# Kernel optimization log

Measured on AMD Instinct MI355X. Metric: run time of the kernel, lower is better.

## Reference

```python
import jax, jax.numpy as jnp
import numpy as np

N_NODES = 50000
N_REL = 3
N_EDGES = 800000
D_FEAT = 128
D_HID = 128  # == dim_embs so residual + concat dims line up
D_QUERY = 64


def setup_inputs() -> dict:
    key = jax.random.key(0)
    ks = jax.random.split(key, 8)
    s = 1.0 / np.sqrt(D_HID)
    return {
        "x": jax.random.normal(ks[0], (N_NODES, D_FEAT), dtype=jnp.float32),
        "edges": jax.random.randint(ks[1], (N_REL, 2, N_EDGES), 0, N_NODES, dtype=jnp.int64),
        "feat_w": jax.random.normal(ks[2], (D_FEAT, D_HID), dtype=jnp.float32) * s,
        "conv_w": jax.random.normal(ks[3], (2, N_REL, D_HID, D_HID), dtype=jnp.float32) * s,
        "conv_b": jax.random.normal(ks[4], (2, N_REL, D_HID), dtype=jnp.float32) * 0.01,
        "attn_w": jax.random.normal(ks[5], (2, D_HID, D_QUERY), dtype=jnp.float32) * s,
        "attn_q": jax.random.normal(ks[6], (2, D_QUERY), dtype=jnp.float32) * s,
        "concat_w": jax.random.normal(ks[7], (D_HID, 3 * D_HID), dtype=jnp.float32) * s,
    }


def reference(x, edges, feat_w, conv_w, conv_b, attn_w, attn_q, concat_w):
    N = x.shape[0]
    R = edges.shape[0]
    ones_e = jnp.ones((edges.shape[2],), dtype=x.dtype)

    def gconv(h, src, dst, W, b):
        # GraphConv with symmetric ('both') normalization + residual
        deg_out = jnp.clip(jax.ops.segment_sum(ones_e, src, num_segments=N), 1.0)
        deg_in = jnp.clip(jax.ops.segment_sum(ones_e, dst, num_segments=N), 1.0)
        m = (h * jax.lax.rsqrt(deg_out)[:, None]) @ W          # [N, D]
        agg = jax.ops.segment_sum(m[src], dst, num_segments=N)  # gather-scatter [E, D] -> [N, D]
        return agg * jax.lax.rsqrt(deg_in)[:, None] + b + h

    def het_layer(h, l):
        # per-relation conv, then attention-weighted aggregation across relations
        vals = jnp.stack([gconv(h, edges[r, 0], edges[r, 1], conv_w[l, r], conv_b[l, r])
                          for r in range(R)])                   # [R, N, D]
        keys = jnp.tanh(jnp.einsum('rnd,dq->rnq', vals, attn_w[l]))
        scores = jnp.einsum('rnq,q->rn', keys, attn_q[l])       # [R, N]
        attn = jax.nn.softmax(scores, axis=0)                   # softmax over relations
        return jnp.einsum('rn,rnd->nd', attn, vals), attn

    h0 = jnp.tanh(x @ feat_w)            # feature_trans + tanh
    h1, _ = het_layer(h0, 1)             # 1-hop path (convs[1] only)
    t, _ = het_layer(h0, 0)              # 2-hop path: convs[0]
    h2, attn = het_layer(t, 1)           # then convs[1]
    y = jnp.concatenate([h0, h1, h2], axis=-1) @ concat_w.T  # concat_weight (no bias)
    return y, attn.T                      # attn_res: [N, R]
```

## Files before the change

kernel.cpp:

```cpp
#include <hip/hip_runtime.h>

#define NN 50000
#define NE 800000
#define DD 128
#define DQ 64
#define NB 42
#define SL 19048
#define NW 25000

typedef __attribute__((ext_vector_type(8))) short short8_t;
typedef __attribute__((ext_vector_type(4))) float f32x4;

__device__ __forceinline__ int clampi(int v, int lo, int hi) {
  return v < lo ? lo : (v > hi ? hi : v);
}
__device__ __forceinline__ unsigned short f2bf(float f) {
  unsigned int u = __float_as_uint(f);
  return (unsigned short)((u + 0x7FFFu + ((u >> 16) & 1u)) >> 16);
}
__device__ __forceinline__ float bfl(unsigned int u) { return __uint_as_float(u << 16); }
__device__ __forceinline__ float bfh(unsigned int u) { return __uint_as_float(u & 0xFFFF0000u); }
__device__ __forceinline__ float b2f(short s) {
  return __uint_as_float(((unsigned int)(unsigned short)s) << 16);
}

__global__ void detect_kernel(const int* __restrict__ e, int* __restrict__ flag) {
  if (threadIdx.x == 0 && blockIdx.x == 0) {
    int f = 1;
    for (int j = 0; j < 32; ++j)
      if (e[2 * j + 1] != 0) f = 0;
    *flag = f;
  }
}

__global__ __launch_bounds__(512) void hist6_kernel(
    const int* __restrict__ e, const int* __restrict__ flag,
    unsigned int* __restrict__ hist) {
  __shared__ unsigned int lds[NW];
  const int b = blockIdx.x;
  const int c = blockIdx.y;
  const int r = c >> 1;
  const int a = c & 1;
  const int tid = threadIdx.x;
  const int f = *flag;
  for (int i = tid; i < NW; i += 512) lds[i] = 0u;
  __syncthreads();
  const long long abase = (long long)r * 2 * NE + (a ? 0 : NE);
  const int beg = b * SL, end = min(beg + SL, NE);
  for (int i = beg + tid; i < end; i += 512) {
    int v = clampi(e[(abase + i) << f], 0, NN - 1);
    atomicAdd(&lds[v >> 1], 1u << ((v & 1) * 16));
  }
  __syncthreads();
  unsigned int* outp = hist + ((size_t)c * NB + b) * NW;
  for (int i = tid; i < NW; i += 512) outp[i] = lds[i];
}

__global__ __launch_bounds__(256) void sumhist_kernel(
    const unsigned int* __restrict__ hist, int* __restrict__ cnt,
    float* __restrict__ rsqi, float* __restrict__ rsqo) {
  const int c = blockIdx.y;
  const int r = c >> 1;
  const int a = c & 1;
  for (int wl = threadIdx.x; wl < 1000; wl += 256) {
    int w = blockIdx.x * 1000 + wl;
    unsigned int lo = 0, hi = 0;
    const unsigned int* hp = hist + (size_t)c * NB * NW + w;
#pragma unroll 7
    for (int b = 0; b < NB; ++b) {
      unsigned int v = hp[(size_t)b * NW];
      lo += v & 0xFFFFu;
      hi += v >> 16;
    }
    int n0 = 2 * w, n1 = 2 * w + 1;
    if (a == 0) {
      cnt[r * NN + n0] = (int)lo;
      cnt[r * NN + n1] = (int)hi;
      rsqi[r * NN + n0] = rsqrtf(fmaxf((float)lo, 1.0f));
      rsqi[r * NN + n1] = rsqrtf(fmaxf((float)hi, 1.0f));
    } else {
      rsqo[r * NN + n0] = rsqrtf(fmaxf((float)lo, 1.0f));
      rsqo[r * NN + n1] = rsqrtf(fmaxf((float)hi, 1.0f));
    }
  }
}

__global__ __launch_bounds__(256) void scanp1_kernel(
    const int* __restrict__ cnt, int* __restrict__ rowptr, int* __restrict__ btot) {
  __shared__ int part[256];
  const int r = blockIdx.y;
  const int b = blockIdx.x;
  const int t = threadIdx.x;
  const int base = b * 2000;
  const int beg = t * 8;
  int v[8];
  int s = 0;
  if (beg < 2000) {
#pragma unroll
    for (int j = 0; j < 8; ++j) {
      v[j] = cnt[r * NN + base + beg + j];
      s += v[j];
    }
  }
  part[t] = s;
  __syncthreads();
  for (int off = 1; off < 256; off <<= 1) {
    int x = (t >= off) ? part[t - off] : 0;
    __syncthreads();
    part[t] += x;
    __syncthreads();
  }
  if (beg < 2000) {
    int excl = part[t] - s;
#pragma unroll
    for (int j = 0; j < 8; ++j) {
      rowptr[r * (NN + 1) + base + beg + j] = excl;
      excl += v[j];
    }
  }
  if (t == 255) btot[r * 25 + b] = part[255];
}

__global__ __launch_bounds__(64) void scanp2_kernel(
    const int* __restrict__ btot, int* __restrict__ boff, int* __restrict__ rowptr) {
  if (threadIdx.x == 0) {
    for (int r = 0; r < 3; ++r) {
      int run = 0;
      for (int b = 0; b < 25; ++b) {
        boff[r * 25 + b] = run;
        run += btot[r * 25 + b];
      }
      rowptr[r * (NN + 1) + NN] = run;
    }
  }
}

__global__ __launch_bounds__(256) void scanp3_kernel(
    const int* __restrict__ boff, int* __restrict__ rowptr) {
  const int r = blockIdx.y, b = blockIdx.x, t = threadIdx.x;
  const int off = boff[r * 25 + b];
  const int beg = t * 8;
  if (beg < 2000) {
    int* rp = rowptr + r * (NN + 1) + b * 2000 + beg;
#pragma unroll
    for (int j = 0; j < 8; ++j) rp[j] += off;
  }
}

__global__ __launch_bounds__(256) void bases_kernel(
    const unsigned int* __restrict__ hist, const int* __restrict__ rowptr,
    int* __restrict__ bases) {
  const int r = blockIdx.y;
  for (int wl = threadIdx.x; wl < 1000; wl += 256) {
    int w = blockIdx.x * 1000 + wl;
    int n0 = 2 * w, n1 = 2 * w + 1;
    int run0 = rowptr[r * (NN + 1) + n0];
    int run1 = rowptr[r * (NN + 1) + n1];
    const unsigned int* hp = hist + (size_t)(r * 2) * NB * NW + w;
    int* bp = bases + (size_t)r * NB * NN;
#pragma unroll 7
    for (int b = 0; b < NB; ++b) {
      unsigned int v = hp[(size_t)b * NW];
      bp[(size_t)b * NN + n0] = run0;
      bp[(size_t)b * NN + n1] = run1;
      run0 += (int)(v & 0xFFFFu);
      run1 += (int)(v >> 16);
    }
  }
}

__global__ __launch_bounds__(512) void fill2_kernel(
    const int* __restrict__ e, const int* __restrict__ flag,
    const int* __restrict__ bases, int* __restrict__ col) {
  __shared__ unsigned int cur[NW];
  const int b = blockIdx.x;
  const int r = blockIdx.y;
  const int tid = threadIdx.x;
  const int f = *flag;
  for (int i = tid; i < NW; i += 512) cur[i] = 0u;
  __syncthreads();
  const long long sbase = (long long)r * 2 * NE;
  const int beg = b * SL, end = min(beg + SL, NE);
  const int* bp = bases + ((size_t)r * NB + b) * NN;
  for (int i = beg + tid; i < end; i += 512) {
    int s = clampi(e[(sbase + i) << f], 0, NN - 1);
    int d = clampi(e[(sbase + NE + i) << f], 0, NN - 1);
    unsigned int packed = atomicAdd(&cur[d >> 1], 1u << ((d & 1) * 16));
    int local = (int)((packed >> ((d & 1) * 16)) & 0xFFFFu);
    int pos = clampi(bp[d] + local, 0, NE - 1);
    col[(size_t)r * NE + pos] = s;
  }
}

__global__ __launch_bounds__(256) void prepw_kernel(
    const float* __restrict__ conv_w, const float* __restrict__ feat_w,
    const float* __restrict__ concat_w, const float* __restrict__ attn_w,
    unsigned short* __restrict__ fw) {
  const int i = blockIdx.x;
  if (i < 10) {
    unsigned short* dst = fw + (size_t)i * 16384;
    for (int e = threadIdx.x; e < 2048; e += 256) {
      int nt = e >> 8, ks = (e >> 6) & 3, lane = e & 63;
      int n = (lane & 15) + nt * 16;
      int kb = (lane >> 4) * 8 + ks * 32;
      unsigned int w[4];
#pragma unroll
      for (int jj = 0; jj < 4; ++jj) {
        int k0 = kb + 2 * jj, k1 = k0 + 1;
        float f0, f1;
        if (i < 6) {
          f0 = conv_w[(size_t)i * 16384 + (size_t)k0 * DD + n];
          f1 = conv_w[(size_t)i * 16384 + (size_t)k1 * DD + n];
        } else if (i == 6) {
          f0 = feat_w[(size_t)k0 * DD + n];
          f1 = feat_w[(size_t)k1 * DD + n];
        } else {
          int p = i - 7;
          f0 = concat_w[(size_t)n * 384 + p * DD + k0];
          f1 = concat_w[(size_t)n * 384 + p * DD + k1];
        }
        w[jj] = (unsigned int)f2bf(f0) | ((unsigned int)f2bf(f1) << 16);
      }
      ((uint4*)dst)[e] = make_uint4(w[0], w[1], w[2], w[3]);
    }
  } else {
    const int l = i - 10;
    unsigned short* dst = fw + (size_t)10 * 16384 + (size_t)l * 8192;
    for (int e = threadIdx.x; e < 1024; e += 256) {
      int nt = e >> 8, ks = (e >> 6) & 3, lane = e & 63;
      int n = (lane & 15) + nt * 16;
      int kb = (lane >> 4) * 8 + ks * 32;
      unsigned int w[4];
#pragma unroll
      for (int jj = 0; jj < 4; ++jj) {
        int k0 = kb + 2 * jj, k1 = k0 + 1;
        float f0 = attn_w[((size_t)l * DD + k0) * DQ + n];
        float f1 = attn_w[((size_t)l * DD + k1) * DQ + n];
        w[jj] = (unsigned int)f2bf(f0) | ((unsigned int)f2bf(f1) << 16);
      }
      ((uint4*)dst)[e] = make_uint4(w[0], w[1], w[2], w[3]);
    }
  }
}

template <int AFP32, int TANH, int EPI, int SIX>
__global__ __launch_bounds__(256) void mgemm_kernel(
    const void* __restrict__ Ap, const unsigned short* __restrict__ fw,
    const float* __restrict__ rsqi, const float* __restrict__ bias,
    const unsigned short* __restrict__ residb, unsigned short* __restrict__ Cb) {
  const size_t ND = (size_t)NN * DD;
  const int rel = blockIdx.y;
  const int wsel = SIX ? (rel + 3) % 6 : rel;
  const int arel = SIX ? rel % 3 : rel;
  const unsigned short* fwp = fw + (size_t)wsel * 16384;
  const float* rsqip = EPI ? rsqi + (size_t)arel * NN : nullptr;
  const float* biasp = EPI ? bias + (size_t)wsel * DD : nullptr;
  unsigned short* Cbp = Cb + (size_t)rel * ND;
  __shared__ unsigned short sF[16384];
  const int tid = threadIdx.x;
  {
    const float4* s = (const float4*)fwp;
    float4* d = (float4*)sF;
#pragma unroll
    for (int i = 0; i < 8; ++i) d[tid + i * 256] = s[tid + i * 256];
  }
  __syncthreads();
  const int w = tid >> 6, l = tid & 63, la = l & 15, gr = l >> 4;
  const int row0 = blockIdx.x * 128 + w * 32;
  if (row0 >= NN) return;
  const bool m1ok = (row0 + 32) <= NN;
  short8_t a[2][4];
#pragma unroll
  for (int m = 0; m < 2; ++m) {
    const int r = row0 + m * 16 + la;
    const bool ok = (m == 0) || m1ok;
    if (AFP32) {
      const float* ap = (const float*)Ap + (size_t)r * DD + gr * 8;
#pragma unroll
      for (int ks = 0; ks < 4; ++ks) {
        short8_t v = (short8_t)0;
        if (ok) {
          float4 x0 = *(const float4*)(ap + ks * 32);
          float4 x1 = *(const float4*)(ap + ks * 32 + 4);
          v[0] = (short)f2bf(x0.x); v[1] = (short)f2bf(x0.y);
          v[2] = (short)f2bf(x0.z); v[3] = (short)f2bf(x0.w);
          v[4] = (short)f2bf(x1.x); v[5] = (short)f2bf(x1.y);
          v[6] = (short)f2bf(x1.z); v[7] = (short)f2bf(x1.w);
        }
        a[m][ks] = v;
      }
    } else {
      const unsigned short* ap =
          (const unsigned short*)Ap + (size_t)arel * ND + (size_t)r * DD + gr * 8;
#pragma unroll
      for (int ks = 0; ks < 4; ++ks)
        a[m][ks] = ok ? *(const short8_t*)(ap + ks * 32) : (short8_t)0;
    }
  }
  f32x4 zero = {0.f, 0.f, 0.f, 0.f};
  f32x4 acc[2][8];
#pragma unroll
  for (int m = 0; m < 2; ++m)
#pragma unroll
    for (int nt = 0; nt < 8; ++nt) acc[m][nt] = zero;
#pragma unroll
  for (int nt = 0; nt < 8; ++nt) {
#pragma unroll
    for (int ks = 0; ks < 4; ++ks) {
      short8_t b = *(const short8_t*)(sF + ((nt * 4 + ks) * 64 + l) * 8);
      acc[0][nt] = __builtin_amdgcn_mfma_f32_16x16x32_bf16(a[0][ks], b, acc[0][nt], 0, 0, 0);
      acc[1][nt] = __builtin_amdgcn_mfma_f32_16x16x32_bf16(a[1][ks], b, acc[1][nt], 0, 0, 0);
    }
  }
#pragma unroll
  for (int m = 0; m < 2; ++m) {
    if (m == 1 && !m1ok) break;
#pragma unroll
    for (int rr = 0; rr < 4; ++rr) {
      const int row = row0 + m * 16 + gr * 4 + rr;
      const float sc = EPI ? rsqip[row] : 0.0f;
#pragma unroll
      for (int nt = 0; nt < 8; ++nt) {
        const int c0 = nt * 16 + la;
        float v = acc[m][nt][rr];
        if (TANH) v = tanhf(v);
        if (EPI) {
          float rv = __uint_as_float((unsigned int)residb[(size_t)row * DD + c0] << 16);
          v = fmaf(v, sc, biasp[c0] + rv);
        }
        Cbp[(size_t)row * DD + c0] = f2bf(v);
      }
    }
  }
}

__global__ __launch_bounds__(512) void mconcat_kernel(
    const unsigned short* __restrict__ h0b, const unsigned short* __restrict__ h1b,
    const unsigned short* __restrict__ h2b, const unsigned short* __restrict__ fwc,
    float* __restrict__ Y) {
  __shared__ unsigned short sF[3 * 16384];
  const int tid = threadIdx.x;
  {
    const float4* s = (const float4*)fwc;
    float4* d = (float4*)sF;
#pragma unroll
    for (int i = 0; i < 12; ++i) d[tid + i * 512] = s[tid + i * 512];
  }
  __syncthreads();
  const int w = tid >> 6, l = tid & 63, la = l & 15, gr = l >> 4;
  const int row0 = blockIdx.x * 256 + w * 32;
  if (row0 >= NN) return;
  const bool m1ok = (row0 + 32) <= NN;
  const unsigned short* hb[3] = {h0b, h1b, h2b};
  f32x4 zero = {0.f, 0.f, 0.f, 0.f};
  f32x4 acc[2][8];
#pragma unroll
  for (int m = 0; m < 2; ++m)
#pragma unroll
    for (int nt = 0; nt < 8; ++nt) acc[m][nt] = zero;
#pragma unroll
  for (int p = 0; p < 3; ++p) {
    short8_t a[2][4];
#pragma unroll
    for (int m = 0; m < 2; ++m) {
      const int r = row0 + m * 16 + la;
      const bool ok = (m == 0) || m1ok;
      const unsigned short* ap = hb[p] + (size_t)r * DD + gr * 8;
#pragma unroll
      for (int ks = 0; ks < 4; ++ks)
        a[m][ks] = ok ? *(const short8_t*)(ap + ks * 32) : (short8_t)0;
    }
    const unsigned short* sfp = sF + p * 16384;
#pragma unroll
    for (int nt = 0; nt < 8; ++nt) {
#pragma unroll
      for (int ks = 0; ks < 4; ++ks) {
        short8_t b = *(const short8_t*)(sfp + ((nt * 4 + ks) * 64 + l) * 8);
        acc[0][nt] = __builtin_amdgcn_mfma_f32_16x16x32_bf16(a[0][ks], b, acc[0][nt], 0, 0, 0);
        acc[1][nt] = __builtin_amdgcn_mfma_f32_16x16x32_bf16(a[1][ks], b, acc[1][nt], 0, 0, 0);
      }
    }
  }
#pragma unroll
  for (int m = 0; m < 2; ++m) {
    if (m == 1 && !m1ok) break;
#pragma unroll
    for (int rr = 0; rr < 4; ++rr) {
      const int row = row0 + m * 16 + gr * 4 + rr;
#pragma unroll
      for (int nt = 0; nt < 8; ++nt)
        Y[(size_t)row * DD + nt * 16 + la] = acc[m][nt][rr];
    }
  }
}

#define ACC8(A, V, C) \
  A[0] = fmaf(bfl((V).x), (C), A[0]); A[1] = fmaf(bfh((V).x), (C), A[1]); \
  A[2] = fmaf(bfl((V).y), (C), A[2]); A[3] = fmaf(bfh((V).y), (C), A[3]); \
  A[4] = fmaf(bfl((V).z), (C), A[4]); A[5] = fmaf(bfh((V).z), (C), A[5]); \
  A[6] = fmaf(bfl((V).w), (C), A[6]); A[7] = fmaf(bfh((V).w), (C), A[7]);

__global__ __launch_bounds__(256) void gatherb_kernel(
    const unsigned short* __restrict__ hb, const int* __restrict__ rowptr,
    const int* __restrict__ col, const float* __restrict__ rsqo,
    unsigned short* __restrict__ ub) {
  const size_t ND = (size_t)NN * DD;
  const int rel = blockIdx.y;
  rowptr += (size_t)rel * (NN + 1);
  col += (size_t)rel * NE;
  rsqo += (size_t)rel * NN;
  ub += (size_t)rel * ND;
  int gid = blockIdx.x * 256 + threadIdx.x;
  int n = gid >> 4;
  int lane = gid & 15;
  int e0 = clampi(rowptr[n], 0, NE);
  int e1 = clampi(rowptr[n + 1], e0, NE);
  const uint4* h4 = (const uint4*)hb;
  float a[8] = {0, 0, 0, 0, 0, 0, 0, 0}, b[8] = {0, 0, 0, 0, 0, 0, 0, 0};
  float c[8] = {0, 0, 0, 0, 0, 0, 0, 0}, d[8] = {0, 0, 0, 0, 0, 0, 0, 0};
  int e = e0;
  for (; e + 7 < e1; e += 8) {
    int s0 = clampi(col[e], 0, NN - 1), s1 = clampi(col[e + 1], 0, NN - 1);
    int s2 = clampi(col[e + 2], 0, NN - 1), s3 = clampi(col[e + 3], 0, NN - 1);
    int s4 = clampi(col[e + 4], 0, NN - 1), s5 = clampi(col[e + 5], 0, NN - 1);
    int s6 = clampi(col[e + 6], 0, NN - 1), s7 = clampi(col[e + 7], 0, NN - 1);
    float c0 = rsqo[s0], c1 = rsqo[s1], c2 = rsqo[s2], c3 = rsqo[s3];
    float c4 = rsqo[s4], c5 = rsqo[s5], c6 = rsqo[s6], c7 = rsqo[s7];
    uint4 v0 = h4[(size_t)s0 * 16 + lane];
    uint4 v1 = h4[(size_t)s1 * 16 + lane];
    uint4 v2 = h4[(size_t)s2 * 16 + lane];
    uint4 v3 = h4[(size_t)s3 * 16 + lane];
    uint4 v4 = h4[(size_t)s4 * 16 + lane];
    uint4 v5 = h4[(size_t)s5 * 16 + lane];
    uint4 v6 = h4[(size_t)s6 * 16 + lane];
    uint4 v7 = h4[(size_t)s7 * 16 + lane];
    ACC8(a, v0, c0) ACC8(b, v1, c1) ACC8(c, v2, c2) ACC8(d, v3, c3)
    ACC8(a, v4, c4) ACC8(b, v5, c5) ACC8(c, v6, c6) ACC8(d, v7, c7)
  }
  for (; e + 3 < e1; e += 4) {
    int s0 = clampi(col[e], 0, NN - 1), s1 = clampi(col[e + 1], 0, NN - 1);
    int s2 = clampi(col[e + 2], 0, NN - 1), s3 = clampi(col[e + 3], 0, NN - 1);
    float c0 = rsqo[s0], c1 = rsqo[s1], c2 = rsqo[s2], c3 = rsqo[s3];
    uint4 v0 = h4[(size_t)s0 * 16 + lane];
    uint4 v1 = h4[(size_t)s1 * 16 + lane];
    uint4 v2 = h4[(size_t)s2 * 16 + lane];
    uint4 v3 = h4[(size_t)s3 * 16 + lane];
    ACC8(a, v0, c0) ACC8(b, v1, c1) ACC8(c, v2, c2) ACC8(d, v3, c3)
  }
  for (; e < e1; ++e) {
    int s0 = clampi(col[e], 0, NN - 1);
    float c0 = rsqo[s0];
    uint4 v0 = h4[(size_t)s0 * 16 + lane];
    ACC8(a, v0, c0)
  }
#pragma unroll
  for (int j = 0; j < 8; ++j) a[j] += b[j] + c[j] + d[j];
  uint4 o;
  o.x = (unsigned int)f2bf(a[0]) | ((unsigned int)f2bf(a[1]) << 16);
  o.y = (unsigned int)f2bf(a[2]) | ((unsigned int)f2bf(a[3]) << 16);
  o.z = (unsigned int)f2bf(a[4]) | ((unsigned int)f2bf(a[5]) << 16);
  o.w = (unsigned int)f2bf(a[6]) | ((unsigned int)f2bf(a[7]) << 16);
  ((uint4*)ub)[gid] = o;
}

template <int TWO>
__global__ __launch_bounds__(256) void mscomb_kernel(
    const unsigned short* __restrict__ Vb, const unsigned short* __restrict__ faB,
    const float* __restrict__ AQB, unsigned short* __restrict__ houtB,
    float* __restrict__ attn_out) {
  const size_t ND = (size_t)NN * DD;
  const int y = TWO ? blockIdx.y : 0;
  const unsigned short* Vp = Vb + (TWO ? (size_t)y * 3 * ND : 0);
  const unsigned short* fa = TWO ? faB + (size_t)(1 - y) * 8192 : faB;
  const float* AQ = TWO ? AQB + (size_t)(1 - y) * DQ : AQB;
  unsigned short* houtb = TWO ? houtB + (size_t)y * ND : houtB;
  __shared__ unsigned short sF[8192];
  __shared__ float sS[4][3][32];
  const int tid = threadIdx.x;
  {
    const float4* s = (const float4*)fa;
    float4* d = (float4*)sF;
#pragma unroll
    for (int i = 0; i < 4; ++i) d[tid + i * 256] = s[tid + i * 256];
  }
  const int w = tid >> 6, l = tid & 63, la = l & 15, gr = l >> 4;
  int row0 = blockIdx.x * 128 + w * 32;
  if (row0 + 32 > NN) row0 = NN - 32;
  short8_t a[3][2][4];
#pragma unroll
  for (int r3 = 0; r3 < 3; ++r3) {
#pragma unroll
    for (int m = 0; m < 2; ++m) {
      const unsigned short* rp =
          Vp + (size_t)r3 * ND + (size_t)(row0 + m * 16 + la) * DD + gr * 8;
#pragma unroll
      for (int ks = 0; ks < 4; ++ks)
        a[r3][m][ks] = *(const short8_t*)(rp + ks * 32);
    }
  }
  __syncthreads();
  float q[4];
#pragma unroll
  for (int nt = 0; nt < 4; ++nt) q[nt] = AQ[la + nt * 16];
#pragma unroll
  for (int r3 = 0; r3 < 3; ++r3) {
    f32x4 zero = {0.f, 0.f, 0.f, 0.f};
    f32x4 acc[2][4];
#pragma unroll
    for (int m = 0; m < 2; ++m)
#pragma unroll
      for (int nt = 0; nt < 4; ++nt) acc[m][nt] = zero;
#pragma unroll
    for (int nt = 0; nt < 4; ++nt) {
#pragma unroll
      for (int ks = 0; ks < 4; ++ks) {
        short8_t b = *(const short8_t*)(sF + ((nt * 4 + ks) * 64 + l) * 8);
        acc[0][nt] = __builtin_amdgcn_mfma_f32_16x16x32_bf16(a[r3][0][ks], b, acc[0][nt], 0, 0, 0);
        acc[1][nt] = __builtin_amdgcn_mfma_f32_16x16x32_bf16(a[r3][1][ks], b, acc[1][nt], 0, 0, 0);
      }
    }
#pragma unroll
    for (int m = 0; m < 2; ++m) {
#pragma unroll
      for (int rr = 0; rr < 4; ++rr) {
        float p = tanhf(acc[m][0][rr]) * q[0] + tanhf(acc[m][1][rr]) * q[1] +
                  tanhf(acc[m][2][rr]) * q[2] + tanhf(acc[m][3][rr]) * q[3];
#pragma unroll
        for (int off = 1; off < 16; off <<= 1) p += __shfl_xor(p, off, 16);
        if (la == 0) sS[w][r3][m * 16 + gr * 4 + rr] = p;
      }
    }
  }
  __syncthreads();
#pragma unroll
  for (int m = 0; m < 2; ++m) {
    const int row = row0 + m * 16 + la;
    float s0 = sS[w][0][m * 16 + la];
    float s1 = sS[w][1][m * 16 + la];
    float s2 = sS[w][2][m * 16 + la];
    float mx = fmaxf(s0, fmaxf(s1, s2));
    float e0 = __expf(s0 - mx), e1 = __expf(s1 - mx), e2 = __expf(s2 - mx);
    float inv = 1.0f / (e0 + e1 + e2);
    float a0 = e0 * inv, a1 = e1 * inv, a2 = e2 * inv;
#pragma unroll
    for (int ks = 0; ks < 4; ++ks) {
      unsigned int ow[4];
#pragma unroll
      for (int jj = 0; jj < 4; ++jj) {
        float v0 = a0 * b2f(a[0][m][ks][2 * jj]) + a1 * b2f(a[1][m][ks][2 * jj]) +
                   a2 * b2f(a[2][m][ks][2 * jj]);
        float v1 = a0 * b2f(a[0][m][ks][2 * jj + 1]) + a1 * b2f(a[1][m][ks][2 * jj + 1]) +
                   a2 * b2f(a[2][m][ks][2 * jj + 1]);
        ow[jj] = (unsigned int)f2bf(v0) | ((unsigned int)f2bf(v1) << 16);
      }
      *(uint4*)(houtb + (size_t)row * DD + gr * 8 + ks * 32) =
          make_uint4(ow[0], ow[1], ow[2], ow[3]);
    }
    if (attn_out != nullptr) {
      attn_out[(size_t)row * 3 + 0] = a0;
      attn_out[(size_t)row * 3 + 1] = a1;
      attn_out[(size_t)row * 3 + 2] = a2;
    }
  }
}

extern "C" void kernel_launch(void* const* d_in, const int* in_sizes, int n_in,
                              void* d_out, int out_size, void* d_ws, size_t ws_size,
                              hipStream_t stream) {
  const float* x        = (const float*)d_in[0];
  const int*   edges    = (const int*)d_in[1];
  const float* feat_w   = (const float*)d_in[2];
  const float* conv_w   = (const float*)d_in[3];
  const float* conv_b   = (const float*)d_in[4];
  const float* attn_w   = (const float*)d_in[5];
  const float* attn_q   = (const float*)d_in[6];
  const float* concat_w = (const float*)d_in[7];
  float* out = (float*)d_out;

  float* ws = (float*)d_ws;
  float* rsqo = ws;
  float* rsqi = rsqo + 3 * NN;
  int* flag = (int*)(rsqi + 3 * NN);
  int* btot = flag + 16;
  int* boff = btot + 80;
  int* cnt = boff + 80;
  int* rowptr = cnt + 3 * NN;
  int* col = rowptr + 3 * (NN + 1) + 13;
  const size_t ND = (size_t)NN * DD;
  float* P1 = (float*)(col + 3 * (size_t)NE);
  float* PA = P1 + ND;
  float* PB = PA + ND;
  unsigned short* U0 = (unsigned short*)(PB + ND);
  unsigned short* B0 = U0 + 3 * ND;
  unsigned short* B1 = B0 + ND;
  unsigned short* B2 = B1 + ND;
  unsigned short* fw = (unsigned short*)cnt;
  unsigned int* hist = (unsigned int*)PA;
  int* bases = (int*)PB;
  unsigned short* VbAll = (unsigned short*)P1;
  unsigned short* fa0 = fw + (size_t)10 * 16384;
  unsigned short* fa1 = fa0 + 8192;

  detect_kernel<<<1, 64, 0, stream>>>(edges, flag);
  hist6_kernel<<<dim3(NB, 6), 512, 0, stream>>>(edges, flag, hist);
  sumhist_kernel<<<dim3(25, 6), 256, 0, stream>>>(hist, cnt, rsqi, rsqo);
  scanp1_kernel<<<dim3(25, 3), 256, 0, stream>>>(cnt, rowptr, btot);
  scanp2_kernel<<<1, 64, 0, stream>>>(btot, boff, rowptr);
  scanp3_kernel<<<dim3(25, 3), 256, 0, stream>>>(boff, rowptr);
  prepw_kernel<<<12, 256, 0, stream>>>(conv_w, feat_w, concat_w, attn_w, fw);
  bases_kernel<<<dim3(25, 3), 256, 0, stream>>>(hist, rowptr, bases);
  fill2_kernel<<<dim3(NB, 3), 512, 0, stream>>>(edges, flag, bases, col);

  mgemm_kernel<1, 1, 0, 0><<<dim3(391, 1), 256, 0, stream>>>(
      x, fw + (size_t)6 * 16384, nullptr, nullptr, nullptr, B0);

  gatherb_kernel<<<dim3(3125, 3), 256, 0, stream>>>(B0, rowptr, col, rsqo, U0);

  mgemm_kernel<0, 0, 1, 1><<<dim3(391, 6), 256, 0, stream>>>(
      U0, fw, rsqi, conv_b, B0, VbAll);
  mscomb_kernel<1><<<dim3(391, 2), 256, 0, stream>>>(
      VbAll, fa0, attn_q, B1, nullptr);

  gatherb_kernel<<<dim3(3125, 3), 256, 0, stream>>>(B2, rowptr, col, rsqo, U0);
  mgemm_kernel<0, 0, 1, 0><<<dim3(391, 3), 256, 0, stream>>>(
      U0, fw + (size_t)3 * 16384, rsqi, conv_b + (size_t)3 * DD, B2, VbAll);
  mscomb_kernel<0><<<dim3(391, 1), 256, 0, stream>>>(
      VbAll, fa1, attn_q + DQ, U0, out + ND);

  mconcat_kernel<<<196, 512, 0, stream>>>(B0, B1, U0, fw + (size_t)7 * 16384, out);
}
```

Before: 465.1 us.

## Record per-edge ranks in histogram pass and fuse CSR build kernels

The destination-histogram pass now also stores each edge's within-block rank, taken from the LDS atomic's return value. This lets the CSR fill become a fully parallel, atomic-free scatter instead of a second LDS-atomic pass over the edges. The histogram reduction is fused with the first scan phase, and the block-offset add is folded into the bases kernel, which removes two launches. The int64 edge-layout detection kernel is dropped, so the code now assumes int32 edge indices. The cost is an extra rank array written and read through global memory.

Result: faster. 453.0 us (-2.6%).

```diff
diff --git a/kernel.cpp b/kernel.cpp
--- a/kernel.cpp
+++ b/kernel.cpp
@@ -24,84 +24,76 @@
   return __uint_as_float(((unsigned int)(unsigned short)s) << 16);
 }
 
-__global__ void detect_kernel(const int* __restrict__ e, int* __restrict__ flag) {
-  if (threadIdx.x == 0 && blockIdx.x == 0) {
-    int f = 1;
-    for (int j = 0; j < 32; ++j)
-      if (e[2 * j + 1] != 0) f = 0;
-    *flag = f;
-  }
-}
-
 __global__ __launch_bounds__(512) void hist6_kernel(
-    const int* __restrict__ e, const int* __restrict__ flag,
-    unsigned int* __restrict__ hist) {
+    const int* __restrict__ e, unsigned int* __restrict__ hist,
+    unsigned short* __restrict__ rank) {
   __shared__ unsigned int lds[NW];
   const int b = blockIdx.x;
   const int c = blockIdx.y;
   const int r = c >> 1;
   const int a = c & 1;
   const int tid = threadIdx.x;
-  const int f = *flag;
   for (int i = tid; i < NW; i += 512) lds[i] = 0u;
   __syncthreads();
-  const long long abase = (long long)r * 2 * NE + (a ? 0 : NE);
+  const size_t abase = (size_t)r * 2 * NE + (a ? 0 : NE);
   const int beg = b * SL, end = min(beg + SL, NE);
-  for (int i = beg + tid; i < end; i += 512) {
-    int v = clampi(e[(abase + i) << f], 0, NN - 1);
-    atomicAdd(&lds[v >> 1], 1u << ((v & 1) * 16));
+  if (a == 0) {
+    unsigned short* rk = rank + (size_t)r * NE;
+    for (int i = beg + tid; i < end; i += 512) {
+      int v = clampi(e[abase + i], 0, NN - 1);
+      unsigned int sh = (v & 1) * 16;
+      unsigned int old = atomicAdd(&lds[v >> 1], 1u << sh);
+      rk[i] = (unsigned short)((old >> sh) & 0xFFFFu);
+    }
+  } else {
+    for (int i = beg + tid; i < end; i += 512) {
+      int v = clampi(e[abase + i], 0, NN - 1);
+      atomicAdd(&lds[v >> 1], 1u << ((v & 1) * 16));
+    }
   }
   __syncthreads();
   unsigned int* outp = hist + ((size_t)c * NB + b) * NW;
   for (int i = tid; i < NW; i += 512) outp[i] = lds[i];
 }
 
-__global__ __launch_bounds__(256) void sumhist_kernel(
-    const unsigned int* __restrict__ hist, int* __restrict__ cnt,
-    float* __restrict__ rsqi, float* __restrict__ rsqo) {
+__global__ __launch_bounds__(256) void sumscan_kernel(
+    const unsigned int* __restrict__ hist, int* __restrict__ rowptr,
+    int* __restrict__ btot, float* __restrict__ rsqi, float* __restrict__ rsqo) {
+  __shared__ int part[256];
+  const int g = blockIdx.x;
   const int c = blockIdx.y;
-  const int r = c >> 1;
-  const int a = c & 1;
-  for (int wl = threadIdx.x; wl < 1000; wl += 256) {
-    int w = blockIdx.x * 1000 + wl;
-    unsigned int lo = 0, hi = 0;
-    const unsigned int* hp = hist + (size_t)c * NB * NW + w;
+  const int r = c >> 1, a = c & 1;
+  const int t = threadIdx.x;
+  int cntv[8];
+  int s = 0;
+  const int w0 = g * 1000 + t * 4;
+  if (t < 250) {
+#pragma unroll
+    for (int j = 0; j < 4; ++j) {
+      const unsigned int* hp = hist + (size_t)c * NB * NW + w0 + j;
+      unsigned int lo = 0, hi = 0;
 #pragma unroll 7
-    for (int b = 0; b < NB; ++b) {
-      unsigned int v = hp[(size_t)b * NW];
-      lo += v & 0xFFFFu;
-      hi += v >> 16;
-    }
-    int n0 = 2 * w, n1 = 2 * w + 1;
-    if (a == 0) {
-      cnt[r * NN + n0] = (int)lo;
-      cnt[r * NN + n1] = (int)hi;
-      rsqi[r * NN + n0] = rsqrtf(fmaxf((float)lo, 1.0f));
-      rsqi[r * NN + n1] = rsqrtf(fmaxf((float)hi, 1.0f));
-    } else {
-      rsqo[r * NN + n0] = rsqrtf(fmaxf((float)lo, 1.0f));
-      rsqo[r * NN + n1] = rsqrtf(fmaxf((float)hi, 1.0f));
-    }
-  }
-}
-
-__global__ __launch_bounds__(256) void scanp1_kernel(
-    const int* __restrict__ cnt, int* __restrict__ rowptr, int* __restrict__ btot) {
-  __shared__ int part[256];
-  const int r = blockIdx.y;
-  const int b = blockIdx.x;
-  const int t = threadIdx.x;
-  const int base = b * 2000;
-  const int beg = t * 8;
-  int v[8];
-  int s = 0;
-  if (beg < 2000) {
-#pragma unroll
-    for (int j = 0; j < 8; ++j) {
-      v[j] = cnt[r * NN + base + beg + j];
-      s += v[j];
-    }
-  }
+      for (int b = 0; b < NB; ++b) {
+        unsigned int v = hp[(size_t)b * NW];
+        lo += v & 0xFFFFu;
+        hi += v >> 16;
+      }
+      cntv[2 * j] = (int)lo;
+      cntv[2 * j + 1] = (int)hi;
+      int n0 = 2 * (w0 + j), n1 = n0 + 1;
+      float f0 = rsqrtf(fmaxf((float)lo, 1.0f));
+      float f1 = rsqrtf(fmaxf((float)hi, 1.0f));
+      if (a == 0) {
+        rsqi[r * NN + n0] = f0;
+        rsqi[r * NN + n1] = f1;
+      } else {
+        rsqo[r * NN + n0] = f0;
+        rsqo[r * NN + n1] = f1;
+      }
+      s += (int)(lo + hi);
+    }
+  }
+  if (a == 1) return;
   part[t] = s;
   __syncthreads();
   for (int off = 1; off < 256; off <<= 1) {
@@ -110,15 +102,16 @@
     part[t] += x;
     __syncthreads();
   }
-  if (beg < 2000) {
+  if (t < 250) {
     int excl = part[t] - s;
+    int base = g * 2000 + t * 8;
 #pragma unroll
     for (int j = 0; j < 8; ++j) {
-      rowptr[r * (NN + 1) + base + beg + j] = excl;
-      excl += v[j];
-    }
-  }
-  if (t == 255) btot[r * 25 + b] = part[255];
+      rowptr[r * (NN + 1) + base + j] = excl;
+      excl += cntv[j];
+    }
+  }
+  if (t == 255) btot[r * 25 + g] = part[255];
 }
 
 __global__ __launch_bounds__(64) void scanp2_kernel(
@@ -135,27 +128,18 @@
   }
 }
 
-__global__ __launch_bounds__(256) void scanp3_kernel(
-    const int* __restrict__ boff, int* __restrict__ rowptr) {
-  const int r = blockIdx.y, b = blockIdx.x, t = threadIdx.x;
-  const int off = boff[r * 25 + b];
-  const int beg = t * 8;
-  if (beg < 2000) {
-    int* rp = rowptr + r * (NN + 1) + b * 2000 + beg;
-#pragma unroll
-    for (int j = 0; j < 8; ++j) rp[j] += off;
-  }
-}
-
 __global__ __launch_bounds__(256) void bases_kernel(
-    const unsigned int* __restrict__ hist, const int* __restrict__ rowptr,
-    int* __restrict__ bases) {
+    const unsigned int* __restrict__ hist, const int* __restrict__ boff,
+    int* __restrict__ rowptr, int* __restrict__ bases) {
   const int r = blockIdx.y;
+  const int off = boff[r * 25 + blockIdx.x];
   for (int wl = threadIdx.x; wl < 1000; wl += 256) {
     int w = blockIdx.x * 1000 + wl;
-    int n0 = 2 * w, n1 = 2 * w + 1;
-    int run0 = rowptr[r * (NN + 1) + n0];
-    int run1 = rowptr[r * (NN + 1) + n1];
+    int n0 = 2 * w, n1 = n0 + 1;
+    int run0 = rowptr[r * (NN + 1) + n0] + off;
+    int run1 = rowptr[r * (NN + 1) + n1] + off;
+    rowptr[r * (NN + 1) + n0] = run0;
+    rowptr[r * (NN + 1) + n1] = run1;
     const unsigned int* hp = hist + (size_t)(r * 2) * NB * NW + w;
     int* bp = bases + (size_t)r * NB * NN;
 #pragma unroll 7
@@ -169,27 +153,18 @@
   }
 }
 
-__global__ __launch_bounds__(512) void fill2_kernel(
-    const int* __restrict__ e, const int* __restrict__ flag,
+__global__ __launch_bounds__(256) void fillr_kernel(
+    const int* __restrict__ e, const unsigned short* __restrict__ rank,
     const int* __restrict__ bases, int* __restrict__ col) {
-  __shared__ unsigned int cur[NW];
-  const int b = blockIdx.x;
   const int r = blockIdx.y;
-  const int tid = threadIdx.x;
-  const int f = *flag;
-  for (int i = tid; i < NW; i += 512) cur[i] = 0u;
-  __syncthreads();
-  const long long sbase = (long long)r * 2 * NE;
-  const int beg = b * SL, end = min(beg + SL, NE);
-  const int* bp = bases + ((size_t)r * NB + b) * NN;
-  for (int i = beg + tid; i < end; i += 512) {
-    int s = clampi(e[(sbase + i) << f], 0, NN - 1);
-    int d = clampi(e[(sbase + NE + i) << f], 0, NN - 1);
-    unsigned int packed = atomicAdd(&cur[d >> 1], 1u << ((d & 1) * 16));
-    int local = (int)((packed >> ((d & 1) * 16)) & 0xFFFFu);
-    int pos = clampi(bp[d] + local, 0, NE - 1);
-    col[(size_t)r * NE + pos] = s;
-  }
+  const int i = blockIdx.x * 256 + threadIdx.x;
+  const size_t sbase = (size_t)r * 2 * NE;
+  int s = clampi(e[sbase + i], 0, NN - 1);
+  int d = clampi(e[sbase + NE + i], 0, NN - 1);
+  int b = i / SL;
+  int pos = clampi(bases[((size_t)r * NB + b) * NN + d] + (int)rank[(size_t)r * NE + i],
+                   0, NE - 1);
+  col[(size_t)r * NE + pos] = s;
 }
 
 __global__ __launch_bounds__(256) void prepw_kernel(
@@ -580,10 +555,9 @@
   float* ws = (float*)d_ws;
   float* rsqo = ws;
   float* rsqi = rsqo + 3 * NN;
-  int* flag = (int*)(rsqi + 3 * NN);
-  int* btot = flag + 16;
+  int* btot = (int*)(rsqi + 3 * NN);
   int* boff = btot + 80;
-  int* cnt = boff + 80;
+  int* cnt = boff + 96;
   int* rowptr = cnt + 3 * NN;
   int* col = rowptr + 3 * (NN + 1) + 13;
   const size_t ND = (size_t)NN * DD;
@@ -597,19 +571,17 @@
   unsigned short* fw = (unsigned short*)cnt;
   unsigned int* hist = (unsigned int*)PA;
   int* bases = (int*)PB;
+  unsigned short* rank = (unsigned short*)P1;
   unsigned short* VbAll = (unsigned short*)P1;
   unsigned short* fa0 = fw + (size_t)10 * 16384;
   unsigned short* fa1 = fa0 + 8192;
 
-  detect_kernel<<<1, 64, 0, stream>>>(edges, flag);
-  hist6_kernel<<<dim3(NB, 6), 512, 0, stream>>>(edges, flag, hist);
-  sumhist_kernel<<<dim3(25, 6), 256, 0, stream>>>(hist, cnt, rsqi, rsqo);
-  scanp1_kernel<<<dim3(25, 3), 256, 0, stream>>>(cnt, rowptr, btot);
+  hist6_kernel<<<dim3(NB, 6), 512, 0, stream>>>(edges, hist, rank);
+  sumscan_kernel<<<dim3(25, 6), 256, 0, stream>>>(hist, rowptr, btot, rsqi, rsqo);
   scanp2_kernel<<<1, 64, 0, stream>>>(btot, boff, rowptr);
-  scanp3_kernel<<<dim3(25, 3), 256, 0, stream>>>(boff, rowptr);
   prepw_kernel<<<12, 256, 0, stream>>>(conv_w, feat_w, concat_w, attn_w, fw);
-  bases_kernel<<<dim3(25, 3), 256, 0, stream>>>(hist, rowptr, bases);
-  fill2_kernel<<<dim3(NB, 3), 512, 0, stream>>>(edges, flag, bases, col);
+  bases_kernel<<<dim3(25, 3), 256, 0, stream>>>(hist, boff, rowptr, bases);
+  fillr_kernel<<<dim3(3125, 3), 256, 0, stream>>>(edges, rank, bases, col);
 
   mgemm_kernel<1, 1, 0, 0><<<dim3(391, 1), 256, 0, stream>>>(
       x, fw + (size_t)6 * 16384, nullptr, nullptr, nullptr, B0);
```
